# Optimization experiments

Hardware: AMD Instinct MI355X
Metric: run time of the kernel (lower is better)

The kernel has to match this reference:

```python
import jax, jax.numpy as jnp
import numpy as np

B, C, T = 32, 256, 4096

def setup_inputs() -> dict:
    key = jax.random.key(0)
    k1, k2 = jax.random.split(key)
    x = jax.random.normal(k1, (B, C, T), dtype=jnp.float32)
    gamma = jax.random.normal(k2, (1,), dtype=jnp.float32)
    return {"x": x, "gamma": gamma}

def reference(x, gamma):
    # energy[b,i,j] = <x[b,i,:], x[b,j,:]>  -> (B, C, C)
    energy = jnp.einsum('bit,bjt->bij', x, x)
    # max-subtract trick: softmax over (rowmax - energy)
    energy_new = jnp.max(energy, axis=-1, keepdims=True) - energy
    attention = jax.nn.softmax(energy_new, axis=-1)
    # out[b,i,t] = sum_j attention[b,i,j] * x[b,j,t]
    out = jnp.einsum('bij,bjt->bit', attention, x)
    return gamma * out + x
```

## Files before the change

kernel.cpp:

```cpp
#include <hip/hip_runtime.h>
#include <hip/hip_bf16.h>

#define BATCH 32
#define CDIM  256
#define TDIM  4096

using short8  = __attribute__((ext_vector_type(8))) short;
using floatx4 = __attribute__((ext_vector_type(4))) float;

__device__ __forceinline__ unsigned f2bf(float f) {
  unsigned u = __float_as_uint(f);
  return (u + 0x7fffu + ((u >> 16) & 1u)) >> 16;
}
__device__ __forceinline__ unsigned cvt_pk_bf16(float a, float b) {
  return f2bf(a) | (f2bf(b) << 16);
}
__device__ __forceinline__ float bf_lo(unsigned u) { return __uint_as_float(u << 16); }
__device__ __forceinline__ float bf_hi(unsigned u) { return __uint_as_float(u & 0xffff0000u); }

__global__ __launch_bounds__(256, 2)
void gram_kernel(const float* __restrict__ x,
                 float* __restrict__ E1, float* __restrict__ E2) {
  __shared__ __align__(16) short hI[64 * 40];
  __shared__ __align__(16) short lI[64 * 40];
  __shared__ __align__(16) short hJ[64 * 40];

  const int tid = threadIdx.x;
  const int bx  = blockIdx.x;
  const int b   = bx >> 4;
  const int i0  = ((bx >> 2) & 3) * 64;
  const int j0  = (bx & 3) * 64;

  const float* xb = x + ((size_t)b << 20);

  const int srow = tid >> 2;
  const int skq  = (tid & 3) << 3;
  const float* pI = xb + (size_t)(i0 + srow) * TDIM + skq;
  const float* pJ = xb + (size_t)(j0 + srow) * TDIM + skq;

  floatx4 acc_hh[2][2], acc_lh[2][2];
#pragma unroll
  for (int m = 0; m < 2; ++m)
#pragma unroll
    for (int n = 0; n < 2; ++n) {
      acc_hh[m][n] = {0.f, 0.f, 0.f, 0.f};
      acc_lh[m][n] = {0.f, 0.f, 0.f, 0.f};
    }

  const int lane = tid & 63;
  const int w    = tid >> 6;
  const int wm   = (w >> 1) << 5;
  const int wn   = (w & 1) << 5;
  const int fr   = lane & 15;
  const int q    = lane >> 4;

  const int aoff0 = (wm + fr) * 40 + q * 8;
  const int aoff1 = aoff0 + 16 * 40;
  const int boff0 = (wn + fr) * 40 + q * 8;
  const int boff1 = boff0 + 16 * 40;

  float4 rI0 = *(const float4*)pI;
  float4 rI1 = *(const float4*)(pI + 4);
  float4 rJ0 = *(const float4*)pJ;
  float4 rJ1 = *(const float4*)(pJ + 4);

  for (int ks = 0; ks < TDIM / 32; ++ks) {
    unsigned hi01 = cvt_pk_bf16(rI0.x, rI0.y), hi23 = cvt_pk_bf16(rI0.z, rI0.w);
    unsigned hi45 = cvt_pk_bf16(rI1.x, rI1.y), hi67 = cvt_pk_bf16(rI1.z, rI1.w);
    unsigned li01 = cvt_pk_bf16(rI0.x - bf_lo(hi01), rI0.y - bf_hi(hi01));
    unsigned li23 = cvt_pk_bf16(rI0.z - bf_lo(hi23), rI0.w - bf_hi(hi23));
    unsigned li45 = cvt_pk_bf16(rI1.x - bf_lo(hi45), rI1.y - bf_hi(hi45));
    unsigned li67 = cvt_pk_bf16(rI1.z - bf_lo(hi67), rI1.w - bf_hi(hi67));
    unsigned hj01 = cvt_pk_bf16(rJ0.x, rJ0.y), hj23 = cvt_pk_bf16(rJ0.z, rJ0.w);
    unsigned hj45 = cvt_pk_bf16(rJ1.x, rJ1.y), hj67 = cvt_pk_bf16(rJ1.z, rJ1.w);

    __syncthreads();
    *(uint4*)(&hI[srow * 40 + skq]) = make_uint4(hi01, hi23, hi45, hi67);
    *(uint4*)(&lI[srow * 40 + skq]) = make_uint4(li01, li23, li45, li67);
    *(uint4*)(&hJ[srow * 40 + skq]) = make_uint4(hj01, hj23, hj45, hj67);
    __syncthreads();

    if (ks < TDIM / 32 - 1) {
      pI += 32; pJ += 32;
      rI0 = *(const float4*)pI; rI1 = *(const float4*)(pI + 4);
      rJ0 = *(const float4*)pJ; rJ1 = *(const float4*)(pJ + 4);
    }

    short8 Ah0 = *(const short8*)(&hI[aoff0]);
    short8 Ah1 = *(const short8*)(&hI[aoff1]);
    short8 Al0 = *(const short8*)(&lI[aoff0]);
    short8 Al1 = *(const short8*)(&lI[aoff1]);
    short8 Bh0 = *(const short8*)(&hJ[boff0]);
    short8 Bh1 = *(const short8*)(&hJ[boff1]);

    acc_hh[0][0] = __builtin_amdgcn_mfma_f32_16x16x32_bf16(Ah0, Bh0, acc_hh[0][0], 0, 0, 0);
    acc_hh[0][1] = __builtin_amdgcn_mfma_f32_16x16x32_bf16(Ah0, Bh1, acc_hh[0][1], 0, 0, 0);
    acc_hh[1][0] = __builtin_amdgcn_mfma_f32_16x16x32_bf16(Ah1, Bh0, acc_hh[1][0], 0, 0, 0);
    acc_hh[1][1] = __builtin_amdgcn_mfma_f32_16x16x32_bf16(Ah1, Bh1, acc_hh[1][1], 0, 0, 0);
    acc_lh[0][0] = __builtin_amdgcn_mfma_f32_16x16x32_bf16(Al0, Bh0, acc_lh[0][0], 0, 0, 0);
    acc_lh[0][1] = __builtin_amdgcn_mfma_f32_16x16x32_bf16(Al0, Bh1, acc_lh[0][1], 0, 0, 0);
    acc_lh[1][0] = __builtin_amdgcn_mfma_f32_16x16x32_bf16(Al1, Bh0, acc_lh[1][0], 0, 0, 0);
    acc_lh[1][1] = __builtin_amdgcn_mfma_f32_16x16x32_bf16(Al1, Bh1, acc_lh[1][1], 0, 0, 0);
  }

#pragma unroll
  for (int m = 0; m < 2; ++m)
#pragma unroll
    for (int n = 0; n < 2; ++n) {
      const int gr = i0 + wm + 16 * m + 4 * q;
      const int gc = j0 + wn + 16 * n + fr;
      size_t base = (((size_t)b * CDIM + gr) << 8) + gc;
#pragma unroll
      for (int r = 0; r < 4; ++r) {
        E1[base + ((size_t)r << 8)] = acc_hh[m][n][r];
        E2[base + ((size_t)r << 8)] = acc_lh[m][n][r];
      }
    }
}

__global__ __launch_bounds__(256)
void softmax_kernel(const float* __restrict__ E1, const float* __restrict__ E2,
                    __hip_bfloat16* __restrict__ att) {
  const int b = blockIdx.x >> 8;
  const int i = blockIdx.x & 255;
  const int j = threadIdx.x;
  const size_t base = (size_t)b << 16;

  float e = E1[base + (i << 8) + j] + E2[base + (i << 8) + j] + E2[base + (j << 8) + i];
  float z = -e;

  float m = z;
#pragma unroll
  for (int off = 32; off > 0; off >>= 1) m = fmaxf(m, __shfl_xor(m, off, 64));

  __shared__ float red[8];
  const int wv = j >> 6, ln = j & 63;
  if (ln == 0) red[wv] = m;
  __syncthreads();
  m = fmaxf(fmaxf(red[0], red[1]), fmaxf(red[2], red[3]));

  float p = expf(z - m);
  float s = p;
#pragma unroll
  for (int off = 32; off > 0; off >>= 1) s += __shfl_xor(s, off, 64);
  if (ln == 0) red[4 + wv] = s;
  __syncthreads();
  s = (red[4] + red[5]) + (red[6] + red[7]);

  att[base + (i << 8) + j] = __float2bfloat16(p / s);
}

__global__ __launch_bounds__(256, 2)
void pv_kernel(const float* __restrict__ x, const __hip_bfloat16* __restrict__ att,
               const float* __restrict__ gamma, float* __restrict__ out) {
  __shared__ __align__(16) short As[128 * 40];
  __shared__ __align__(16) short Bt[128 * 40];

  const int tid = threadIdx.x;
  const int bx  = blockIdx.x;
  const int b   = bx >> 6;
  const int i0  = ((bx >> 5) & 1) << 7;
  const int t0  = (bx & 31) << 7;

  const float* xb = x + ((size_t)b << 20);
  const unsigned short* attb = (const unsigned short*)att + ((size_t)b << 16);

  const int arow = tid >> 1;
  const int aoff = (tid & 1) << 4;
  const int kg = tid >> 5;
  const int tg = tid & 31;

  floatx4 acc[4][4];
#pragma unroll
  for (int m = 0; m < 4; ++m)
#pragma unroll
    for (int n = 0; n < 4; ++n) acc[m][n] = {0.f, 0.f, 0.f, 0.f};

  const int lane = tid & 63;
  const int w    = tid >> 6;
  const int wm   = (w >> 1) << 6;
  const int wn   = (w & 1) << 6;
  const int fr   = lane & 15;
  const int q    = lane >> 4;

  const unsigned short* pA = attb + (size_t)(i0 + arow) * CDIM + aoff;
  const float* pB = xb + (size_t)(kg * 4) * TDIM + t0 + tg;

  uint4 ra0 = *(const uint4*)pA;
  uint4 ra1 = *(const uint4*)(pA + 8);
  float xv[4][4];
#pragma unroll
  for (int kk = 0; kk < 4; ++kk)
#pragma unroll
    for (int tt = 0; tt < 4; ++tt) xv[kk][tt] = pB[kk * TDIM + tt * 32];

  for (int ks = 0; ks < CDIM / 32; ++ks) {
    unsigned bu[4][2];
#pragma unroll
    for (int tt = 0; tt < 4; ++tt) {
      bu[tt][0] = cvt_pk_bf16(xv[0][tt], xv[1][tt]);
      bu[tt][1] = cvt_pk_bf16(xv[2][tt], xv[3][tt]);
    }

    __syncthreads();
    *(uint4*)(&As[arow * 40 + aoff])     = ra0;
    *(uint4*)(&As[arow * 40 + aoff + 8]) = ra1;
#pragma unroll
    for (int tt = 0; tt < 4; ++tt)
      *(uint2*)(&Bt[(tg + tt * 32) * 40 + kg * 4]) = make_uint2(bu[tt][0], bu[tt][1]);
    __syncthreads();

    if (ks < CDIM / 32 - 1) {
      pA += 32; pB += (size_t)32 * TDIM;
      ra0 = *(const uint4*)pA;
      ra1 = *(const uint4*)(pA + 8);
#pragma unroll
      for (int kk = 0; kk < 4; ++kk)
#pragma unroll
        for (int tt = 0; tt < 4; ++tt) xv[kk][tt] = pB[kk * TDIM + tt * 32];
    }

    short8 Af[4], Bf[4];
#pragma unroll
    for (int m = 0; m < 4; ++m) Af[m] = *(const short8*)(&As[(wm + 16 * m + fr) * 40 + q * 8]);
#pragma unroll
    for (int n = 0; n < 4; ++n) Bf[n] = *(const short8*)(&Bt[(wn + 16 * n + fr) * 40 + q * 8]);
#pragma unroll
    for (int m = 0; m < 4; ++m)
#pragma unroll
      for (int n = 0; n < 4; ++n)
        acc[m][n] = __builtin_amdgcn_mfma_f32_16x16x32_bf16(Af[m], Bf[n], acc[m][n], 0, 0, 0);
  }

  const float g = gamma[0];
#pragma unroll
  for (int m = 0; m < 4; ++m)
#pragma unroll
    for (int n = 0; n < 4; ++n) {
      const int gr = i0 + wm + 16 * m + 4 * q;
      const int gc = t0 + wn + 16 * n + fr;
      size_t base = ((size_t)b << 20) + (size_t)gr * TDIM + gc;
#pragma unroll
      for (int r = 0; r < 4; ++r) {
        size_t idx = base + (size_t)r * TDIM;
        out[idx] = g * acc[m][n][r] + x[idx];
      }
    }
}

extern "C" void kernel_launch(void* const* d_in, const int* in_sizes, int n_in,
                              void* d_out, int out_size, void* d_ws, size_t ws_size,
                              hipStream_t stream) {
  (void)in_sizes; (void)n_in; (void)out_size; (void)ws_size;
  const float* x     = (const float*)d_in[0];
  const float* gamma = (const float*)d_in[1];
  float* out = (float*)d_out;

  const size_t EN = (size_t)BATCH * CDIM * CDIM;
  float* E1 = (float*)d_ws;
  float* E2 = E1 + EN;
  __hip_bfloat16* att = (__hip_bfloat16*)(E2 + EN);

  gram_kernel<<<dim3(512), dim3(256), 0, stream>>>(x, E1, E2);
  softmax_kernel<<<dim3(BATCH * CDIM), dim3(256), 0, stream>>>(E1, E2, att);
  pv_kernel<<<dim3(2048), dim3(256), 0, stream>>>(x, att, gamma, out);
}
```

Before: 410.4 us.

## Exploit Gram symmetry with split-K 128x128 tiles and atomic accumulation

```diff
diff --git a/kernel.cpp b/kernel.cpp
--- a/kernel.cpp
+++ b/kernel.cpp
@@ -4,6 +4,10 @@
 #define BATCH 32
 #define CDIM  256
 #define TDIM  4096
+#define SPLIT 8
+#define KCH   (TDIM / SPLIT)
+#define BK    32
+#define NIT   (KCH / BK)
 
 using short8  = __attribute__((ext_vector_type(8))) short;
 using floatx4 = __attribute__((ext_vector_type(4))) float;
@@ -18,116 +22,165 @@
 __device__ __forceinline__ float bf_lo(unsigned u) { return __uint_as_float(u << 16); }
 __device__ __forceinline__ float bf_hi(unsigned u) { return __uint_as_float(u & 0xffff0000u); }
 
+__device__ __forceinline__ void cvt4(const float4 v, unsigned& h0, unsigned& h1,
+                                     unsigned& l0, unsigned& l1) {
+  h0 = cvt_pk_bf16(v.x, v.y);
+  h1 = cvt_pk_bf16(v.z, v.w);
+  l0 = cvt_pk_bf16(v.x - bf_lo(h0), v.y - bf_hi(h0));
+  l1 = cvt_pk_bf16(v.z - bf_lo(h1), v.w - bf_hi(h1));
+}
+
 __global__ __launch_bounds__(256, 2)
-void gram_kernel(const float* __restrict__ x,
-                 float* __restrict__ E1, float* __restrict__ E2) {
-  __shared__ __align__(16) short hI[64 * 40];
-  __shared__ __align__(16) short lI[64 * 40];
-  __shared__ __align__(16) short hJ[64 * 40];
-
-  const int tid = threadIdx.x;
-  const int bx  = blockIdx.x;
-  const int b   = bx >> 4;
-  const int i0  = ((bx >> 2) & 3) * 64;
-  const int j0  = (bx & 3) * 64;
+void gram_sym(const float* __restrict__ x, float* __restrict__ energy) {
+  __shared__ __align__(16) char smem[4 * 128 * 40 * 2];
+  short* hIs = (short*)smem;
+  short* lIs = hIs + 128 * 40;
+  short* hJs = lIs + 128 * 40;
+  short* lJs = hJs + 128 * 40;
+  float* tbuf = (float*)smem;
+
+  const int tid  = threadIdx.x;
+  const int bx   = blockIdx.x;
+  const int b    = bx / (3 * SPLIT);
+  const int rem  = bx % (3 * SPLIT);
+  const int tile = rem / SPLIT;
+  const int kc   = rem % SPLIT;
+  const bool diag = (tile < 2);
+  const int I0 = (tile == 1) ? 128 : 0;
+  const int J0 = (tile == 0) ? 0 : 128;
 
   const float* xb = x + ((size_t)b << 20);
-
-  const int srow = tid >> 2;
-  const int skq  = (tid & 3) << 3;
-  const float* pI = xb + (size_t)(i0 + srow) * TDIM + skq;
-  const float* pJ = xb + (size_t)(j0 + srow) * TDIM + skq;
-
-  floatx4 acc_hh[2][2], acc_lh[2][2];
-#pragma unroll
-  for (int m = 0; m < 2; ++m)
-#pragma unroll
-    for (int n = 0; n < 2; ++n) {
-      acc_hh[m][n] = {0.f, 0.f, 0.f, 0.f};
-      acc_lh[m][n] = {0.f, 0.f, 0.f, 0.f};
-    }
+  float* eb = energy + ((size_t)b << 16);
+
+  const int srow = tid >> 1;
+  const int scol = (tid & 1) << 4;
+  const float* pI = xb + (size_t)(I0 + srow) * TDIM + kc * KCH + scol;
+  const float* pJ = xb + (size_t)(J0 + srow) * TDIM + kc * KCH + scol;
+
+  floatx4 acc[4][4];
+#pragma unroll
+  for (int m = 0; m < 4; ++m)
+#pragma unroll
+    for (int n = 0; n < 4; ++n) acc[m][n] = {0.f, 0.f, 0.f, 0.f};
 
   const int lane = tid & 63;
   const int w    = tid >> 6;
-  const int wm   = (w >> 1) << 5;
-  const int wn   = (w & 1) << 5;
+  const int wm   = (w >> 1) << 6;
+  const int wn   = (w & 1) << 6;
   const int fr   = lane & 15;
   const int q    = lane >> 4;
 
-  const int aoff0 = (wm + fr) * 40 + q * 8;
-  const int aoff1 = aoff0 + 16 * 40;
-  const int boff0 = (wn + fr) * 40 + q * 8;
-  const int boff1 = boff0 + 16 * 40;
-
-  float4 rI0 = *(const float4*)pI;
-  float4 rI1 = *(const float4*)(pI + 4);
-  float4 rJ0 = *(const float4*)pJ;
-  float4 rJ1 = *(const float4*)(pJ + 4);
-
-  for (int ks = 0; ks < TDIM / 32; ++ks) {
-    unsigned hi01 = cvt_pk_bf16(rI0.x, rI0.y), hi23 = cvt_pk_bf16(rI0.z, rI0.w);
-    unsigned hi45 = cvt_pk_bf16(rI1.x, rI1.y), hi67 = cvt_pk_bf16(rI1.z, rI1.w);
-    unsigned li01 = cvt_pk_bf16(rI0.x - bf_lo(hi01), rI0.y - bf_hi(hi01));
-    unsigned li23 = cvt_pk_bf16(rI0.z - bf_lo(hi23), rI0.w - bf_hi(hi23));
-    unsigned li45 = cvt_pk_bf16(rI1.x - bf_lo(hi45), rI1.y - bf_hi(hi45));
-    unsigned li67 = cvt_pk_bf16(rI1.z - bf_lo(hi67), rI1.w - bf_hi(hi67));
-    unsigned hj01 = cvt_pk_bf16(rJ0.x, rJ0.y), hj23 = cvt_pk_bf16(rJ0.z, rJ0.w);
-    unsigned hj45 = cvt_pk_bf16(rJ1.x, rJ1.y), hj67 = cvt_pk_bf16(rJ1.z, rJ1.w);
+  float4 rI[4], rJ[4];
+#pragma unroll
+  for (int u = 0; u < 4; ++u) rI[u] = *(const float4*)(pI + 4 * u);
+  if (!diag) {
+#pragma unroll
+    for (int u = 0; u < 4; ++u) rJ[u] = *(const float4*)(pJ + 4 * u);
+  }
+
+  for (int ks = 0; ks < NIT; ++ks) {
+    unsigned hw[8], lw[8], hwj[8], lwj[8];
+#pragma unroll
+    for (int u = 0; u < 4; ++u)
+      cvt4(rI[u], hw[2 * u], hw[2 * u + 1], lw[2 * u], lw[2 * u + 1]);
+    if (!diag) {
+#pragma unroll
+      for (int u = 0; u < 4; ++u)
+        cvt4(rJ[u], hwj[2 * u], hwj[2 * u + 1], lwj[2 * u], lwj[2 * u + 1]);
+    }
 
     __syncthreads();
-    *(uint4*)(&hI[srow * 40 + skq]) = make_uint4(hi01, hi23, hi45, hi67);
-    *(uint4*)(&lI[srow * 40 + skq]) = make_uint4(li01, li23, li45, li67);
-    *(uint4*)(&hJ[srow * 40 + skq]) = make_uint4(hj01, hj23, hj45, hj67);
+    *(uint4*)&hIs[srow * 40 + scol]     = make_uint4(hw[0], hw[1], hw[2], hw[3]);
+    *(uint4*)&hIs[srow * 40 + scol + 8] = make_uint4(hw[4], hw[5], hw[6], hw[7]);
+    *(uint4*)&lIs[srow * 40 + scol]     = make_uint4(lw[0], lw[1], lw[2], lw[3]);
+    *(uint4*)&lIs[srow * 40 + scol + 8] = make_uint4(lw[4], lw[5], lw[6], lw[7]);
+    if (!diag) {
+      *(uint4*)&hJs[srow * 40 + scol]     = make_uint4(hwj[0], hwj[1], hwj[2], hwj[3]);
+      *(uint4*)&hJs[srow * 40 + scol + 8] = make_uint4(hwj[4], hwj[5], hwj[6], hwj[7]);
+      *(uint4*)&lJs[srow * 40 + scol]     = make_uint4(lwj[0], lwj[1], lwj[2], lwj[3]);
+      *(uint4*)&lJs[srow * 40 + scol + 8] = make_uint4(lwj[4], lwj[5], lwj[6], lwj[7]);
+    }
     __syncthreads();
 
-    if (ks < TDIM / 32 - 1) {
-      pI += 32; pJ += 32;
-      rI0 = *(const float4*)pI; rI1 = *(const float4*)(pI + 4);
-      rJ0 = *(const float4*)pJ; rJ1 = *(const float4*)(pJ + 4);
-    }
-
-    short8 Ah0 = *(const short8*)(&hI[aoff0]);
-    short8 Ah1 = *(const short8*)(&hI[aoff1]);
-    short8 Al0 = *(const short8*)(&lI[aoff0]);
-    short8 Al1 = *(const short8*)(&lI[aoff1]);
-    short8 Bh0 = *(const short8*)(&hJ[boff0]);
-    short8 Bh1 = *(const short8*)(&hJ[boff1]);
-
-    acc_hh[0][0] = __builtin_amdgcn_mfma_f32_16x16x32_bf16(Ah0, Bh0, acc_hh[0][0], 0, 0, 0);
-    acc_hh[0][1] = __builtin_amdgcn_mfma_f32_16x16x32_bf16(Ah0, Bh1, acc_hh[0][1], 0, 0, 0);
-    acc_hh[1][0] = __builtin_amdgcn_mfma_f32_16x16x32_bf16(Ah1, Bh0, acc_hh[1][0], 0, 0, 0);
-    acc_hh[1][1] = __builtin_amdgcn_mfma_f32_16x16x32_bf16(Ah1, Bh1, acc_hh[1][1], 0, 0, 0);
-    acc_lh[0][0] = __builtin_amdgcn_mfma_f32_16x16x32_bf16(Al0, Bh0, acc_lh[0][0], 0, 0, 0);
-    acc_lh[0][1] = __builtin_amdgcn_mfma_f32_16x16x32_bf16(Al0, Bh1, acc_lh[0][1], 0, 0, 0);
-    acc_lh[1][0] = __builtin_amdgcn_mfma_f32_16x16x32_bf16(Al1, Bh0, acc_lh[1][0], 0, 0, 0);
-    acc_lh[1][1] = __builtin_amdgcn_mfma_f32_16x16x32_bf16(Al1, Bh1, acc_lh[1][1], 0, 0, 0);
+    if (ks < NIT - 1) {
+      pI += BK;
+#pragma unroll
+      for (int u = 0; u < 4; ++u) rI[u] = *(const float4*)(pI + 4 * u);
+      if (!diag) {
+        pJ += BK;
+#pragma unroll
+        for (int u = 0; u < 4; ++u) rJ[u] = *(const float4*)(pJ + 4 * u);
+      }
+    }
+
+    const short* hB = diag ? hIs : hJs;
+    const short* lB = diag ? lIs : lJs;
+
+    short8 Ah[4], Al[4], Bh[4], Bl[4];
+#pragma unroll
+    for (int m = 0; m < 4; ++m) {
+      Ah[m] = *(const short8*)&hIs[(wm + 16 * m + fr) * 40 + q * 8];
+      Al[m] = *(const short8*)&lIs[(wm + 16 * m + fr) * 40 + q * 8];
+    }
+#pragma unroll
+    for (int n = 0; n < 4; ++n) {
+      Bh[n] = *(const short8*)&hB[(wn + 16 * n + fr) * 40 + q * 8];
+      Bl[n] = *(const short8*)&lB[(wn + 16 * n + fr) * 40 + q * 8];
+    }
+#pragma unroll
+    for (int m = 0; m < 4; ++m)
+#pragma unroll
+      for (int n = 0; n < 4; ++n) {
+        acc[m][n] = __builtin_amdgcn_mfma_f32_16x16x32_bf16(Ah[m], Bh[n], acc[m][n], 0, 0, 0);
+        acc[m][n] = __builtin_amdgcn_mfma_f32_16x16x32_bf16(Al[m], Bh[n], acc[m][n], 0, 0, 0);
+        acc[m][n] = __builtin_amdgcn_mfma_f32_16x16x32_bf16(Ah[m], Bl[n], acc[m][n], 0, 0, 0);
+      }
   }
 
 #pragma unroll
-  for (int m = 0; m < 2; ++m)
-#pragma unroll
-    for (int n = 0; n < 2; ++n) {
-      const int gr = i0 + wm + 16 * m + 4 * q;
-      const int gc = j0 + wn + 16 * n + fr;
-      size_t base = (((size_t)b * CDIM + gr) << 8) + gc;
-#pragma unroll
-      for (int r = 0; r < 4; ++r) {
-        E1[base + ((size_t)r << 8)] = acc_hh[m][n][r];
-        E2[base + ((size_t)r << 8)] = acc_lh[m][n][r];
-      }
-    }
+  for (int m = 0; m < 4; ++m)
+#pragma unroll
+    for (int n = 0; n < 4; ++n) {
+      const int gr = I0 + wm + 16 * m + 4 * q;
+      const int gc = J0 + wn + 16 * n + fr;
+#pragma unroll
+      for (int r = 0; r < 4; ++r)
+        atomicAdd(&eb[((gr + r) << 8) + gc], acc[m][n][r]);
+    }
+
+  if (!diag) {
+#pragma unroll
+    for (int h = 0; h < 2; ++h) {
+      __syncthreads();
+      if (wm == (h << 6)) {
+#pragma unroll
+        for (int m = 0; m < 4; ++m)
+#pragma unroll
+          for (int n = 0; n < 4; ++n)
+#pragma unroll
+            for (int r = 0; r < 4; ++r)
+              tbuf[(16 * m + 4 * q + r) * 129 + wn + 16 * n + fr] = acc[m][n][r];
+      }
+      __syncthreads();
+      const int jr = tid >> 1;
+      const int cb = (tid & 1) << 5;
+#pragma unroll
+      for (int k2 = 0; k2 < 32; ++k2) {
+        float v = tbuf[(cb + k2) * 129 + jr];
+        atomicAdd(&eb[((J0 + jr) << 8) + I0 + (h << 6) + cb + k2], v);
+      }
+    }
+  }
 }
 
 __global__ __launch_bounds__(256)
-void softmax_kernel(const float* __restrict__ E1, const float* __restrict__ E2,
-                    __hip_bfloat16* __restrict__ att) {
+void softmax_kernel(const float* __restrict__ energy, __hip_bfloat16* __restrict__ att) {
   const int b = blockIdx.x >> 8;
   const int i = blockIdx.x & 255;
   const int j = threadIdx.x;
   const size_t base = (size_t)b << 16;
 
-  float e = E1[base + (i << 8) + j] + E2[base + (i << 8) + j] + E2[base + (j << 8) + i];
-  float z = -e;
+  float z = -energy[base + (i << 8) + j];
 
   float m = z;
 #pragma unroll
@@ -257,11 +310,11 @@
   float* out = (float*)d_out;
 
   const size_t EN = (size_t)BATCH * CDIM * CDIM;
-  float* E1 = (float*)d_ws;
-  float* E2 = E1 + EN;
-  __hip_bfloat16* att = (__hip_bfloat16*)(E2 + EN);
-
-  gram_kernel<<<dim3(512), dim3(256), 0, stream>>>(x, E1, E2);
-  softmax_kernel<<<dim3(BATCH * CDIM), dim3(256), 0, stream>>>(E1, E2, att);
+  float* energy = (float*)d_ws;
+  __hip_bfloat16* att = (__hip_bfloat16*)(energy + EN);
+
+  hipMemsetAsync(energy, 0, EN * sizeof(float), stream);
+  gram_sym<<<dim3(BATCH * 3 * SPLIT), dim3(256), 0, stream>>>(x, energy);
+  softmax_kernel<<<dim3(BATCH * CDIM), dim3(256), 0, stream>>>(energy, att);
   pv_kernel<<<dim3(2048), dim3(256), 0, stream>>>(x, att, gamma, out);
 }
```

Result: slower. 524.8 us (+27.9%).
